# Kernel tuning notes

Hardware: AMD Instinct MI355X
Metric: run time of the kernel (lower is better)

The kernel has to match this reference:

```python
import jax, jax.numpy as jnp
import numpy as np

NUM_HEADS = 16
BLOCK = 64  # block_size = min(64, N)

def setup_inputs() -> dict:
    key = jax.random.key(0)
    k0, k1, k2 = jax.random.split(key, 3)
    B, N, C = 2, 2048, 1024
    x = jax.random.normal(k0, (B, N, C), dtype=jnp.float32)
    w_qkv = jax.random.normal(k1, (3 * C, C), dtype=jnp.float32) * 0.02  # torch Linear weight [out,in]
    w_proj = jax.random.normal(k2, (C, C), dtype=jnp.float32) * 0.02
    b_proj = jnp.zeros((C,), dtype=jnp.float32)
    return {"x": x, "w_qkv": w_qkv, "w_proj": w_proj, "b_proj": b_proj}

def reference(x, w_qkv, w_proj, b_proj):
    B, N, C = x.shape
    H = NUM_HEADS
    hd = C // H
    bs = min(BLOCK, N)
    scale = hd ** -0.5
    # qkv projection: [B,N,3C] -> [3,B,H,N,hd]
    qkv = (x @ w_qkv.T).reshape(B, N, 3, H, hd).transpose(2, 0, 3, 1, 4)
    q, k, v = qkv[0], qkv[1], qkv[2]
    # block-causal mask: query block i attends to all key blocks <= i
    blk = jnp.arange(N) // bs
    mask = blk[:, None] >= blk[None, :]  # [N,N]
    scores = jnp.einsum('bhqd,bhkd->bhqk', q, k) * scale
    scores = jnp.where(mask, scores, -jnp.inf)
    weights = jax.nn.softmax(scores, axis=-1)
    out = jnp.einsum('bhqk,bhkd->bhqd', weights, v)
    out = out.transpose(0, 2, 1, 3).reshape(B, N, C)
    return out @ w_proj.T + b_proj
```

## Files before the change

### kernel.cpp

```cpp
#include <hip/hip_runtime.h>

typedef __attribute__((ext_vector_type(8))) short bf16x8;
typedef __attribute__((ext_vector_type(4))) float f32x4;

__device__ __forceinline__ unsigned short f2bf(float f) {
  unsigned int u = __float_as_uint(f);
  u += 0x7fffu + ((u >> 16) & 1u);
  return (unsigned short)(u >> 16);
}

__device__ __forceinline__ void gload_lds16(const unsigned short* g, unsigned short* l) {
  __builtin_amdgcn_global_load_lds(
      (const __attribute__((address_space(1))) unsigned int*)g,
      (__attribute__((address_space(3))) unsigned int*)l,
      16, 0, 0);
}

__global__ void cvt_all(const float* __restrict__ x, const float* __restrict__ wq,
                        const float* __restrict__ wp, unsigned short* __restrict__ dst) {
  const int n1 = 4096 * 1024 / 4, n2 = 3072 * 1024 / 4, n3 = 1024 * 1024 / 4;
  int stride = gridDim.x * blockDim.x;
  for (int i = blockIdx.x * blockDim.x + threadIdx.x; i < n1 + n2 + n3; i += stride) {
    const float* s; int j;
    if (i < n1)           { s = x;  j = i; }
    else if (i < n1 + n2) { s = wq; j = i - n1; }
    else                  { s = wp; j = i - n1 - n2; }
    float4 v = ((const float4*)s)[j];
    ushort4 o;
    o.x = f2bf(v.x); o.y = f2bf(v.y); o.z = f2bf(v.z); o.w = f2bf(v.w);
    ((ushort4*)dst)[i] = o;
  }
}

__device__ __forceinline__ void gemm128_bt(const unsigned short* __restrict__ A,
                                           const unsigned short* __restrict__ Bt,
                                           unsigned short* As, unsigned short* Bs,
                                           int tm, int tn, f32x4 acc[4][4]) {
  const int K = 1024;
  int tid = threadIdx.x;
  int w = tid >> 6, l = tid & 63;
  int wr = w >> 1, wc = w & 1;
  int g = l >> 4, c = l & 15;

  int srow = w * 32 + (l >> 2);
  int skoff = (((l & 3) ^ ((srow >> 1) & 3)) * 8);
  const unsigned short* gA = A + (size_t)(tm * 128 + srow) * K + skoff;
  const unsigned short* gB = Bt + (size_t)(tn * 128 + srow) * K + skoff;
  unsigned short* lA = As + (w * 32) * 32;
  unsigned short* lB = Bs + (w * 32) * 32;

  int rx = (c >> 1) & 3;
  int arow = wr * 64 + c;
  int brow = wc * 64 + c;

  for (int k0 = 0; k0 < K; k0 += 32) {
    gload_lds16(gA, lA);
    gload_lds16(gA + 16 * K, lA + 16 * 32);
    gload_lds16(gB, lB);
    gload_lds16(gB + 16 * K, lB + 16 * 32);
    gA += 32; gB += 32;
    __syncthreads();
    bf16x8 af[4], bfr[4];
#pragma unroll
    for (int mi = 0; mi < 4; ++mi)
      af[mi] = *(const bf16x8*)((const char*)As + (arow + mi * 16) * 64 + ((g ^ rx) << 4));
#pragma unroll
    for (int ni = 0; ni < 4; ++ni)
      bfr[ni] = *(const bf16x8*)((const char*)Bs + (brow + ni * 16) * 64 + ((g ^ rx) << 4));
#pragma unroll
    for (int mi = 0; mi < 4; ++mi)
#pragma unroll
      for (int ni = 0; ni < 4; ++ni)
        acc[mi][ni] = __builtin_amdgcn_mfma_f32_16x16x32_bf16(af[mi], bfr[ni], acc[mi][ni], 0, 0, 0);
    __syncthreads();
  }
}

__global__ __launch_bounds__(256) void qkv_gemm(const unsigned short* __restrict__ xb,
                                                const unsigned short* __restrict__ wb,
                                                unsigned short* __restrict__ Qp,
                                                unsigned short* __restrict__ Kp,
                                                unsigned short* __restrict__ Vt) {
  __shared__ unsigned short As[128 * 32];
  __shared__ unsigned short Bs[128 * 32];
  f32x4 acc[4][4];
#pragma unroll
  for (int i = 0; i < 4; ++i)
#pragma unroll
    for (int j = 0; j < 4; ++j) acc[i][j] = f32x4{0.f, 0.f, 0.f, 0.f};
  int id = (blockIdx.x & 7) * 96 + (blockIdx.x >> 3);
  int tm = id / 24, tn = id % 24;
  gemm128_bt(xb, wb, As, Bs, tm, tn, acc);

  int tid = threadIdx.x;
  int w = tid >> 6, l = tid & 63;
  int wr = w >> 1, wc = w & 1;
  int g = l >> 4, c = l & 15;
  const float QSCALE = 0.125f * 1.44269504088896f;
#pragma unroll
  for (int mi = 0; mi < 4; ++mi)
#pragma unroll
    for (int ni = 0; ni < 4; ++ni)
#pragma unroll
      for (int r = 0; r < 4; ++r) {
        int row = tm * 128 + wr * 64 + mi * 16 + g * 4 + r;
        int col = tn * 128 + wc * 64 + ni * 16 + c;
        int b = row >> 11, seq = row & 2047;
        int t = col >> 10;
        int h = (col >> 6) & 15, d = col & 63;
        size_t bh = (size_t)b * 16 + h;
        float v = acc[mi][ni][r];
        if (t == 0)      Qp[(bh * 2048 + seq) * 64 + d] = f2bf(v * QSCALE);
        else if (t == 1) Kp[(bh * 2048 + seq) * 64 + d] = f2bf(v);
        else             Vt[(bh * 64 + d) * 2048 + seq] = f2bf(v);
      }
}

__global__ __launch_bounds__(256, 3) void attn_fa(const unsigned short* __restrict__ Qp,
                                                  const unsigned short* __restrict__ Kp,
                                                  const unsigned short* __restrict__ Vt,
                                                  unsigned short* __restrict__ attn) {
  __shared__ unsigned short Ks[2][4096];
  __shared__ unsigned short Vs[2][4096];
  __shared__ unsigned short Plds[4][16][72];
  int tid = threadIdx.x;
  int w = tid >> 6, l = tid & 63;
  int g = l >> 4, c = l & 15;

  int idx = blockIdx.x;
  int pos = idx >> 3;
  int qb = 31 - (pos >> 2);
  int bh = (idx & 7) + 8 * (pos & 3);

  const unsigned short* Qbh = Qp + (size_t)bh * 2048 * 64;
  const unsigned short* Kbh = Kp + (size_t)bh * 2048 * 64;
  const unsigned short* Vbh = Vt + (size_t)bh * 64 * 2048;

  int rowA, colA, rowB, colB;
  { int L = tid * 16;         int P = L ^ (((L >> 7) & 7) << 4); rowA = P >> 7; colA = (P & 127) >> 1; }
  { int L = (tid + 256) * 16; int P = L ^ (((L >> 7) & 7) << 4); rowB = P >> 7; colB = (P & 127) >> 1; }
  const unsigned short* gKA = Kbh + rowA * 64 + colA;
  const unsigned short* gKB = Kbh + rowB * 64 + colB;
  const unsigned short* gVA = Vbh + (size_t)rowA * 2048 + colA;
  const unsigned short* gVB = Vbh + (size_t)rowB * 2048 + colB;

#define STAGE(buf, kb)                                              \
  do {                                                              \
    gload_lds16(gKA + (kb) * 4096, &Ks[(buf)][w * 512]);            \
    gload_lds16(gKB + (kb) * 4096, &Ks[(buf)][w * 512 + 2048]);     \
    gload_lds16(gVA + (kb) * 64,  &Vs[(buf)][w * 512]);             \
    gload_lds16(gVB + (kb) * 64,  &Vs[(buf)][w * 512 + 2048]);      \
  } while (0)

  bf16x8 qf[2];
  {
    size_t qrow = (size_t)qb * 64 + w * 16 + c;
    qf[0] = *(const bf16x8*)(Qbh + qrow * 64 + 8 * g);
    qf[1] = *(const bf16x8*)(Qbh + qrow * 64 + 32 + 8 * g);
  }

  float lp[4] = {0.f, 0.f, 0.f, 0.f};
  f32x4 o[4];
#pragma unroll
  for (int df = 0; df < 4; ++df) o[df] = f32x4{0.f, 0.f, 0.f, 0.f};

  int xorv = c & 7;

  int cur = 0;
  STAGE(0, 0);
  __syncthreads();
  for (int kb = 0; kb <= qb; ++kb) {
    if (kb < qb) STAGE(1 - cur, kb + 1);

    const char* Kb = (const char*)&Ks[cur][0];
    const char* Vb = (const char*)&Vs[cur][0];
    bf16x8 kf[8];
#pragma unroll
    for (int nf = 0; nf < 4; ++nf) {
      int r = nf * 16 + c;
#pragma unroll
      for (int ks = 0; ks < 2; ++ks)
        kf[nf * 2 + ks] = *(const bf16x8*)(Kb + r * 128 + (((ks * 4 + g) ^ xorv) * 16));
    }
    f32x4 s4[4];
#pragma unroll
    for (int nf = 0; nf < 4; ++nf) {
      s4[nf] = f32x4{0.f, 0.f, 0.f, 0.f};
      s4[nf] = __builtin_amdgcn_mfma_f32_16x16x32_bf16(qf[0], kf[nf * 2 + 0], s4[nf], 0, 0, 0);
      s4[nf] = __builtin_amdgcn_mfma_f32_16x16x32_bf16(qf[1], kf[nf * 2 + 1], s4[nf], 0, 0, 0);
    }
    bf16x8 vf[8];
#pragma unroll
    for (int df = 0; df < 4; ++df) {
      int r = df * 16 + c;
#pragma unroll
      for (int ks = 0; ks < 2; ++ks)
        vf[df * 2 + ks] = *(const bf16x8*)(Vb + r * 128 + (((ks * 4 + g) ^ xorv) * 16));
    }
#pragma unroll
    for (int nf = 0; nf < 4; ++nf)
#pragma unroll
      for (int r = 0; r < 4; ++r) {
        float p = __builtin_amdgcn_exp2f(s4[nf][r]);
        lp[r] += p;
        Plds[w][g * 4 + r][nf * 16 + c] = f2bf(p);
      }
#pragma unroll
    for (int ks = 0; ks < 2; ++ks) {
      bf16x8 pf = *(const bf16x8*)(&Plds[w][c][ks * 32 + 8 * g]);
#pragma unroll
      for (int df = 0; df < 4; ++df)
        o[df] = __builtin_amdgcn_mfma_f32_16x16x32_bf16(pf, vf[df * 2 + ks], o[df], 0, 0, 0);
    }
    __syncthreads();
    cur ^= 1;
  }
#undef STAGE

#pragma unroll
  for (int mask = 1; mask < 16; mask <<= 1)
#pragma unroll
    for (int r = 0; r < 4; ++r) lp[r] += __shfl_xor(lp[r], mask);
  float inv[4];
#pragma unroll
  for (int r = 0; r < 4; ++r) inv[r] = __builtin_amdgcn_rcpf(lp[r]);

  int b = bh >> 4, h = bh & 15;
#pragma unroll
  for (int df = 0; df < 4; ++df)
#pragma unroll
    for (int r = 0; r < 4; ++r) {
      int row = qb * 64 + w * 16 + g * 4 + r;
      int colc = h * 64 + df * 16 + c;
      attn[((size_t)b * 2048 + row) * 1024 + colc] = f2bf(o[df][r] * inv[r]);
    }
}

__global__ __launch_bounds__(256) void proj_gemm(const unsigned short* __restrict__ attn,
                                                 const unsigned short* __restrict__ wpb,
                                                 const float* __restrict__ bias,
                                                 float* __restrict__ out) {
  __shared__ unsigned short As[128 * 32];
  __shared__ unsigned short Bs[128 * 32];
  f32x4 acc[4][4];
#pragma unroll
  for (int i = 0; i < 4; ++i)
#pragma unroll
    for (int j = 0; j < 4; ++j) acc[i][j] = f32x4{0.f, 0.f, 0.f, 0.f};
  int id = (blockIdx.x & 7) * 32 + (blockIdx.x >> 3);
  int tm = id / 8, tn = id % 8;
  gemm128_bt(attn, wpb, As, Bs, tm, tn, acc);

  int tid = threadIdx.x;
  int w = tid >> 6, l = tid & 63;
  int wr = w >> 1, wc = w & 1;
  int g = l >> 4, c = l & 15;
#pragma unroll
  for (int mi = 0; mi < 4; ++mi)
#pragma unroll
    for (int ni = 0; ni < 4; ++ni)
#pragma unroll
      for (int r = 0; r < 4; ++r) {
        int row = tm * 128 + wr * 64 + mi * 16 + g * 4 + r;
        int col = tn * 128 + wc * 64 + ni * 16 + c;
        out[(size_t)row * 1024 + col] = acc[mi][ni][r] + bias[col];
      }
}

extern "C" void kernel_launch(void* const* d_in, const int* in_sizes, int n_in,
                              void* d_out, int out_size, void* d_ws, size_t ws_size,
                              hipStream_t stream) {
  (void)in_sizes; (void)n_in; (void)out_size; (void)ws_size;
  const float* x      = (const float*)d_in[0];
  const float* w_qkv  = (const float*)d_in[1];
  const float* w_proj = (const float*)d_in[2];
  const float* b_proj = (const float*)d_in[3];
  float* out = (float*)d_out;

  unsigned short* xb    = (unsigned short*)d_ws;
  unsigned short* wqkvb = xb + 4096 * 1024;
  unsigned short* wpb   = wqkvb + 3072 * 1024;
  unsigned short* Qp    = wpb + 1024 * 1024;
  unsigned short* Kp    = Qp + 32 * 2048 * 64;
  unsigned short* Vt    = Kp + 32 * 2048 * 64;
  unsigned short* attn  = Vt + 32 * 64 * 2048;

  cvt_all<<<2048, 256, 0, stream>>>(x, w_qkv, w_proj, xb);
  qkv_gemm<<<768, 256, 0, stream>>>(xb, wqkvb, Qp, Kp, Vt);
  attn_fa<<<1024, 256, 0, stream>>>(Qp, Kp, Vt, attn);
  proj_gemm<<<256, 256, 0, stream>>>(attn, wpb, b_proj, out);
}
```

Before: 112.3 us.

## Keep attention probabilities in registers via transposed QK^T MFMA, drop P LDS round-trip

Swaps the MFMA operand order so S is computed transposed, letting each lane's exp'd probabilities directly form the A operand of a 16x16x16 bf16 MFMA for the PV product. This removes the per-block write and read of P through shared memory and its scalar bf16 conversions, using packed v_cvt_pk_bf16_f32 instead. V is now read as 8-byte fragments matching the smaller MFMA shape, and the row-sum reduction is restructured to use fewer shuffles. The cost is twice as many, smaller PV MFMAs and inline asm that the compiler cannot schedule around.

```diff
diff --git a/kernel.cpp b/kernel.cpp
--- a/kernel.cpp
+++ b/kernel.cpp
@@ -2,6 +2,7 @@
 
 typedef __attribute__((ext_vector_type(8))) short bf16x8;
 typedef __attribute__((ext_vector_type(4))) float f32x4;
+typedef __attribute__((ext_vector_type(2))) unsigned int u32x2;
 
 __device__ __forceinline__ unsigned short f2bf(float f) {
   unsigned int u = __float_as_uint(f);
@@ -122,7 +123,6 @@
                                                   unsigned short* __restrict__ attn) {
   __shared__ unsigned short Ks[2][4096];
   __shared__ unsigned short Vs[2][4096];
-  __shared__ unsigned short Plds[4][16][72];
   int tid = threadIdx.x;
   int w = tid >> 6, l = tid & 63;
   int g = l >> 4, c = l & 15;
@@ -159,7 +159,7 @@
     qf[1] = *(const bf16x8*)(Qbh + qrow * 64 + 32 + 8 * g);
   }
 
-  float lp[4] = {0.f, 0.f, 0.f, 0.f};
+  float lp4[4] = {0.f, 0.f, 0.f, 0.f};
   f32x4 o[4];
 #pragma unroll
   for (int df = 0; df < 4; ++df) o[df] = f32x4{0.f, 0.f, 0.f, 0.f};
@@ -186,44 +186,43 @@
 #pragma unroll
     for (int nf = 0; nf < 4; ++nf) {
       s4[nf] = f32x4{0.f, 0.f, 0.f, 0.f};
-      s4[nf] = __builtin_amdgcn_mfma_f32_16x16x32_bf16(qf[0], kf[nf * 2 + 0], s4[nf], 0, 0, 0);
-      s4[nf] = __builtin_amdgcn_mfma_f32_16x16x32_bf16(qf[1], kf[nf * 2 + 1], s4[nf], 0, 0, 0);
-    }
-    bf16x8 vf[8];
+      s4[nf] = __builtin_amdgcn_mfma_f32_16x16x32_bf16(kf[nf * 2 + 0], qf[0], s4[nf], 0, 0, 0);
+      s4[nf] = __builtin_amdgcn_mfma_f32_16x16x32_bf16(kf[nf * 2 + 1], qf[1], s4[nf], 0, 0, 0);
+    }
+    u32x2 pa[4];
+#pragma unroll
+    for (int nf = 0; nf < 4; ++nf) {
+      float p0 = __builtin_amdgcn_exp2f(s4[nf][0]);
+      float p1 = __builtin_amdgcn_exp2f(s4[nf][1]);
+      float p2 = __builtin_amdgcn_exp2f(s4[nf][2]);
+      float p3 = __builtin_amdgcn_exp2f(s4[nf][3]);
+      lp4[nf] += (p0 + p1) + (p2 + p3);
+      unsigned int w0, w1;
+      asm("v_cvt_pk_bf16_f32 %0, %1, %2" : "=v"(w0) : "v"(p0), "v"(p1));
+      asm("v_cvt_pk_bf16_f32 %0, %1, %2" : "=v"(w1) : "v"(p2), "v"(p3));
+      pa[nf][0] = w0; pa[nf][1] = w1;
+    }
 #pragma unroll
     for (int df = 0; df < 4; ++df) {
-      int r = df * 16 + c;
-#pragma unroll
-      for (int ks = 0; ks < 2; ++ks)
-        vf[df * 2 + ks] = *(const bf16x8*)(Vb + r * 128 + (((ks * 4 + g) ^ xorv) * 16));
-    }
-#pragma unroll
-    for (int nf = 0; nf < 4; ++nf)
-#pragma unroll
-      for (int r = 0; r < 4; ++r) {
-        float p = __builtin_amdgcn_exp2f(s4[nf][r]);
-        lp[r] += p;
-        Plds[w][g * 4 + r][nf * 16 + c] = f2bf(p);
+      int vrow = df * 16 + c;
+#pragma unroll
+      for (int ks = 0; ks < 4; ++ks) {
+        u32x2 vbf = *(const u32x2*)(Vb + vrow * 128 + (((2 * ks + (g >> 1)) ^ xorv) * 16) + 8 * (g & 1));
+        asm("v_mfma_f32_16x16x16_bf16 %0, %1, %2, %0"
+            : "+v"(o[df]) : "v"(pa[ks]), "v"(vbf));
       }
-#pragma unroll
-    for (int ks = 0; ks < 2; ++ks) {
-      bf16x8 pf = *(const bf16x8*)(&Plds[w][c][ks * 32 + 8 * g]);
-#pragma unroll
-      for (int df = 0; df < 4; ++df)
-        o[df] = __builtin_amdgcn_mfma_f32_16x16x32_bf16(pf, vf[df * 2 + ks], o[df], 0, 0, 0);
     }
     __syncthreads();
     cur ^= 1;
   }
 #undef STAGE
 
-#pragma unroll
-  for (int mask = 1; mask < 16; mask <<= 1)
-#pragma unroll
-    for (int r = 0; r < 4; ++r) lp[r] += __shfl_xor(lp[r], mask);
+  float lp = (lp4[0] + lp4[1]) + (lp4[2] + lp4[3]);
+  lp += __shfl_xor(lp, 16);
+  lp += __shfl_xor(lp, 32);
   float inv[4];
 #pragma unroll
-  for (int r = 0; r < 4; ++r) inv[r] = __builtin_amdgcn_rcpf(lp[r]);
+  for (int r = 0; r < 4; ++r) inv[r] = __builtin_amdgcn_rcpf(__shfl(lp, g * 4 + r));
 
   int b = bh >> 4, h = bh & 15;
 #pragma unroll
```

New measurement: 110.0 us. -2.0%, faster.
